# Kernel tuning notes

Measured on AMD Instinct MI355X. Metric: run time of the kernel, lower is better.

Reference implementation:

```python
import jax, jax.numpy as jnp
import numpy as np

N = 8192       # nodes
F = 256        # features
RATIO = 0.5    # fraction of nodes kept
K_KEEP = int(np.ceil(RATIO * N))  # 4096, static for jit
EDGE_PROB = 0.004  # sparse binary adjacency density


def setup_inputs() -> dict:
    key = jax.random.key(0)
    kx, ka, kp = jax.random.split(key, 3)
    X = jax.random.normal(kx, (N, F), dtype=jnp.float32)
    # binary adjacency, ~EDGE_PROB density (layer treats it as dense float)
    A = (jax.random.uniform(ka, (N, N)) < EDGE_PROB).astype(jnp.float32)
    p = jax.random.normal(kp, (F, 1), dtype=jnp.float32)  # learnable kernel
    return {"X": X, "A": A, "p": p}


def reference(X, A, p):
    # y = X p / ||p||  (scores), shape (N, 1)
    p_norm = p / jnp.sqrt(jnp.sum(p * p))
    y = X @ p_norm
    scores = y[:, 0]
    # top-K node indices; boolean_mask in the original preserves original
    # node order, so sort the indices ascending
    _, idx = jax.lax.top_k(scores, K_KEEP)
    idx = jnp.sort(idx)
    # gated features: X * tanh(y), then gather kept rows
    feats = X * jnp.tanh(y)            # (N, F)
    X_pooled = feats[idx]              # (K_KEEP, F)
    # A' = A[idx, idx]
    A_pooled = A[idx][:, idx]          # (K_KEEP, K_KEEP)
    return X_pooled, A_pooled
```

## Files before the change

kernel.cpp:

```cpp
#include <hip/hip_runtime.h>
#include <math.h>
#include <stdint.h>

#define N_ROWS 8192
#define F_DIM  256
#define K_KEEP 4096
#define JCH    512

typedef float nfloat4 __attribute__((ext_vector_type(4)));

#define GLOBAL_LOAD_LDS16(gaddr, laddr)                                          \
    __builtin_amdgcn_global_load_lds(                                            \
        (const __attribute__((address_space(1))) void*)(gaddr),                  \
        (__attribute__((address_space(3))) void*)(laddr), 16, 0, 0)

__global__ void k_scores(const float* __restrict__ X, const float* __restrict__ p,
                         float* __restrict__ s_out, float* __restrict__ t_out,
                         int* __restrict__ rank_arr) {
    const int tid  = threadIdx.x;
    const int wv   = tid >> 6;
    const int lane = tid & 63;
    const int row  = blockIdx.x * 4 + wv;

    const int gid = blockIdx.x * 256 + tid;
    if (gid < N_ROWS) rank_arr[gid] = 0;

    const float4 pv = ((const float4*)p)[lane];
    const float4 xv = ((const float4*)(X + (size_t)row * F_DIM))[lane];

    double d  = (double)xv.x * pv.x + (double)xv.y * pv.y
              + (double)xv.z * pv.z + (double)xv.w * pv.w;
    double pp = (double)pv.x * pv.x + (double)pv.y * pv.y
              + (double)pv.z * pv.z + (double)pv.w * pv.w;

    #pragma unroll
    for (int off = 32; off > 0; off >>= 1) {
        d  += __shfl_down(d, off);
        pp += __shfl_down(pp, off);
    }
    if (lane == 0) {
        double y = d / sqrt(pp);
        s_out[row] = (float)y;
        t_out[row] = tanhf((float)y);
    }
}

__global__ void k_rank(const float* __restrict__ s, int* __restrict__ rank_arr) {
    const int ib = blockIdx.x >> 4;
    const int jc = blockIdx.x & 15;
    __shared__ float sk[JCH];
    const int tid = threadIdx.x;

    #pragma unroll
    for (int k = tid; k < JCH; k += 256) sk[k] = s[jc * JCH + k];
    __syncthreads();

    const int   i     = ib * 256 + tid;
    const float si    = s[i];
    const int   jbase = jc * JCH;
    int cnt = 0;
    #pragma unroll 8
    for (int j = 0; j < JCH; ++j) {
        const float v = sk[j];
        cnt += (v > si) ? 1 : 0;
        cnt += ((v == si) && ((jbase + j) < i)) ? 1 : 0;
    }
    atomicAdd(&rank_arr[i], cnt);
}

__global__ void k_compact(const int* __restrict__ rank_arr, int* __restrict__ idx) {
    const int tid  = threadIdx.x;
    const int lane = tid & 63;
    const int wv   = tid >> 6;

    int4 ra[8];
    #pragma unroll
    for (int k = 0; k < 8; ++k) ra[k] = ((const int4*)rank_arr)[tid * 8 + k];
    const int* r32 = (const int*)ra;

    int c = 0;
    #pragma unroll
    for (int k = 0; k < 32; ++k) c += (r32[k] < K_KEEP) ? 1 : 0;

    int v = c;
    #pragma unroll
    for (int off = 1; off < 64; off <<= 1) {
        int n = __shfl_up(v, off);
        if (lane >= off) v += n;
    }
    __shared__ int wsum[4];
    if (lane == 63) wsum[wv] = v;
    __syncthreads();
    int wbase = 0;
    for (int w = 0; w < wv; ++w) wbase += wsum[w];

    int pos = wbase + v - c;
    const int base = tid * 32;
    #pragma unroll
    for (int k = 0; k < 32; ++k) {
        if (r32[k] < K_KEEP) idx[pos++] = base + k;
    }
}

__global__ __launch_bounds__(256) void k_pool(const float* __restrict__ X,
                                              const float* __restrict__ A,
                                              const float* __restrict__ t,
                                              const int* __restrict__ idx,
                                              float* __restrict__ out0,
                                              float* __restrict__ out1) {
    __shared__ float row[N_ROWS];
    const int tid = threadIdx.x;
    const int r   = blockIdx.x;
    const int src = idx[r];

    const float* Arow = A + (size_t)src * N_ROWS;
    #pragma unroll
    for (int k = 0; k < 8; ++k) {
        const int e = k * 1024 + tid * 4;
        GLOBAL_LOAD_LDS16(Arow + e, &row[e]);
    }

    const float tt = t[src];
    if (tid < 64) {
        float4 v = ((const float4*)(X + (size_t)src * F_DIM))[tid];
        nfloat4 o = {v.x * tt, v.y * tt, v.z * tt, v.w * tt};
        __builtin_nontemporal_store(o, (nfloat4*)(out0 + (size_t)r * F_DIM) + tid);
    }
    __syncthreads();

    float* orow = out1 + (size_t)r * K_KEEP;
    #pragma unroll
    for (int k = 0; k < 16; ++k) {
        const int c  = k * 256 + tid;
        const int ci = idx[c];
        __builtin_nontemporal_store(row[ci], orow + c);
    }
}

extern "C" void kernel_launch(void* const* d_in, const int* in_sizes, int n_in,
                              void* d_out, int out_size, void* d_ws, size_t ws_size,
                              hipStream_t stream) {
    const float* X = (const float*)d_in[0];
    const float* A = (const float*)d_in[1];
    const float* p = (const float*)d_in[2];

    float* ws_f   = (float*)d_ws;
    float* s_arr  = ws_f;
    float* t_arr  = ws_f + N_ROWS;
    int*   rank_a = (int*)(ws_f + 2 * N_ROWS);
    int*   idx    = (int*)(ws_f + 3 * N_ROWS);

    float* out0 = (float*)d_out;
    float* out1 = out0 + (size_t)K_KEEP * F_DIM;

    k_scores <<<N_ROWS / 4, 256, 0, stream>>>(X, p, s_arr, t_arr, rank_a);
    k_rank   <<<32 * 16,    256, 0, stream>>>(s_arr, rank_a);
    k_compact<<<1,          256, 0, stream>>>(rank_a, idx);
    k_pool   <<<K_KEEP,     256, 0, stream>>>(X, A, t_arr, idx, out0, out1);
}
```

Before: 378.8 us.

## Gather A columns directly from global instead of staging full rows in LDS

k_pool no longer copies each entire 32KB A row into shared memory. It gathers the 4096 selected columns straight from global memory with int4 index loads and float4 nontemporal stores, which removes the block barrier. This roughly halves the bytes read from A, since only the kept columns are touched, but it turns the row copy into scattered 4-byte gathers. k_rank is also vectorised with float4 LDS reads, and k_compact now uses 1024 threads with 8 elements each for more parallelism.

```diff
diff --git a/kernel.cpp b/kernel.cpp
--- a/kernel.cpp
+++ b/kernel.cpp
@@ -8,11 +8,6 @@
 #define JCH    512
 
 typedef float nfloat4 __attribute__((ext_vector_type(4)));
-
-#define GLOBAL_LOAD_LDS16(gaddr, laddr)                                          \
-    __builtin_amdgcn_global_load_lds(                                            \
-        (const __attribute__((address_space(1))) void*)(gaddr),                  \
-        (__attribute__((address_space(3))) void*)(laddr), 16, 0, 0)
 
 __global__ void k_scores(const float* __restrict__ X, const float* __restrict__ p,
                          float* __restrict__ s_out, float* __restrict__ t_out,
@@ -51,36 +46,43 @@
     __shared__ float sk[JCH];
     const int tid = threadIdx.x;
 
-    #pragma unroll
-    for (int k = tid; k < JCH; k += 256) sk[k] = s[jc * JCH + k];
+    if (tid < JCH / 4)
+        ((float4*)sk)[tid] = ((const float4*)(s + jc * JCH))[tid];
     __syncthreads();
 
     const int   i     = ib * 256 + tid;
     const float si    = s[i];
     const int   jbase = jc * JCH;
     int cnt = 0;
-    #pragma unroll 8
-    for (int j = 0; j < JCH; ++j) {
-        const float v = sk[j];
-        cnt += (v > si) ? 1 : 0;
-        cnt += ((v == si) && ((jbase + j) < i)) ? 1 : 0;
+    #pragma unroll 4
+    for (int q = 0; q < JCH / 4; ++q) {
+        const float4 v = ((const float4*)sk)[q];
+        const int j0 = jbase + 4 * q;
+        cnt += (v.x > si) ? 1 : 0;
+        cnt += ((v.x == si) && (j0 + 0 < i)) ? 1 : 0;
+        cnt += (v.y > si) ? 1 : 0;
+        cnt += ((v.y == si) && (j0 + 1 < i)) ? 1 : 0;
+        cnt += (v.z > si) ? 1 : 0;
+        cnt += ((v.z == si) && (j0 + 2 < i)) ? 1 : 0;
+        cnt += (v.w > si) ? 1 : 0;
+        cnt += ((v.w == si) && (j0 + 3 < i)) ? 1 : 0;
     }
     atomicAdd(&rank_arr[i], cnt);
 }
 
-__global__ void k_compact(const int* __restrict__ rank_arr, int* __restrict__ idx) {
+__global__ __launch_bounds__(1024) void k_compact(const int* __restrict__ rank_arr,
+                                                  int* __restrict__ idx) {
     const int tid  = threadIdx.x;
     const int lane = tid & 63;
     const int wv   = tid >> 6;
 
-    int4 ra[8];
-    #pragma unroll
-    for (int k = 0; k < 8; ++k) ra[k] = ((const int4*)rank_arr)[tid * 8 + k];
-    const int* r32 = (const int*)ra;
+    const int4 ra0 = ((const int4*)rank_arr)[tid * 2 + 0];
+    const int4 ra1 = ((const int4*)rank_arr)[tid * 2 + 1];
+    int r32[8] = {ra0.x, ra0.y, ra0.z, ra0.w, ra1.x, ra1.y, ra1.z, ra1.w};
 
     int c = 0;
     #pragma unroll
-    for (int k = 0; k < 32; ++k) c += (r32[k] < K_KEEP) ? 1 : 0;
+    for (int k = 0; k < 8; ++k) c += (r32[k] < K_KEEP) ? 1 : 0;
 
     int v = c;
     #pragma unroll
@@ -88,16 +90,16 @@
         int n = __shfl_up(v, off);
         if (lane >= off) v += n;
     }
-    __shared__ int wsum[4];
+    __shared__ int wsum[16];
     if (lane == 63) wsum[wv] = v;
     __syncthreads();
     int wbase = 0;
     for (int w = 0; w < wv; ++w) wbase += wsum[w];
 
     int pos = wbase + v - c;
-    const int base = tid * 32;
+    const int base = tid * 8;
     #pragma unroll
-    for (int k = 0; k < 32; ++k) {
+    for (int k = 0; k < 8; ++k) {
         if (r32[k] < K_KEEP) idx[pos++] = base + k;
     }
 }
@@ -108,17 +110,12 @@
                                               const int* __restrict__ idx,
                                               float* __restrict__ out0,
                                               float* __restrict__ out1) {
-    __shared__ float row[N_ROWS];
     const int tid = threadIdx.x;
     const int r   = blockIdx.x;
     const int src = idx[r];
 
-    const float* Arow = A + (size_t)src * N_ROWS;
-    #pragma unroll
-    for (int k = 0; k < 8; ++k) {
-        const int e = k * 1024 + tid * 4;
-        GLOBAL_LOAD_LDS16(Arow + e, &row[e]);
-    }
+    const float* __restrict__ Arow = A + (size_t)src * N_ROWS;
+    float* __restrict__ orow = out1 + (size_t)r * K_KEEP;
 
     const float tt = t[src];
     if (tid < 64) {
@@ -126,14 +123,13 @@
         nfloat4 o = {v.x * tt, v.y * tt, v.z * tt, v.w * tt};
         __builtin_nontemporal_store(o, (nfloat4*)(out0 + (size_t)r * F_DIM) + tid);
     }
-    __syncthreads();
 
-    float* orow = out1 + (size_t)r * K_KEEP;
     #pragma unroll
-    for (int k = 0; k < 16; ++k) {
-        const int c  = k * 256 + tid;
-        const int ci = idx[c];
-        __builtin_nontemporal_store(row[ci], orow + c);
+    for (int k = 0; k < 4; ++k) {
+        const int c4 = k * 256 + tid;
+        const int4 ci = ((const int4*)idx)[c4];
+        nfloat4 o = {Arow[ci.x], Arow[ci.y], Arow[ci.z], Arow[ci.w]};
+        __builtin_nontemporal_store(o, (nfloat4*)orow + c4);
     }
 }
 
@@ -153,8 +149,8 @@
     float* out0 = (float*)d_out;
     float* out1 = out0 + (size_t)K_KEEP * F_DIM;
 
-    k_scores <<<N_ROWS / 4, 256, 0, stream>>>(X, p, s_arr, t_arr, rank_a);
-    k_rank   <<<32 * 16,    256, 0, stream>>>(s_arr, rank_a);
-    k_compact<<<1,          256, 0, stream>>>(rank_a, idx);
-    k_pool   <<<K_KEEP,     256, 0, stream>>>(X, A, t_arr, idx, out0, out1);
+    k_scores <<<N_ROWS / 4, 256,  0, stream>>>(X, p, s_arr, t_arr, rank_a);
+    k_rank   <<<32 * 16,    256,  0, stream>>>(s_arr, rank_a);
+    k_compact<<<1,          1024, 0, stream>>>(rank_a, idx);
+    k_pool   <<<K_KEEP,     256,  0, stream>>>(X, A, t_arr, idx, out0, out1);
 }
```

Result: no change. 375.8 us (-0.8%).
